# Kernel tuning notes

Measured on AMD Instinct MI355X. Metric: run time of the kernel, lower is better.

Reference implementation:

```python
import jax, jax.numpy as jnp
import numpy as np

M = 0.4
S = 64.0
EPS = 1e-5

def _normalize(x, axis=-1):
    n = jnp.linalg.norm(x, axis=axis, keepdims=True)
    return x / jnp.maximum(n, EPS)

def setup_inputs() -> dict:
    key = jax.random.key(0)
    k1, k2, k3 = jax.random.split(key, 3)
    B, D, C = 512, 512, 100000
    inp = jax.random.normal(k1, (B, D), dtype=jnp.float32)
    weight = jax.random.normal(k2, (C, D), dtype=jnp.float32) * (D ** -0.5)
    label = jax.random.randint(k3, (B,), 0, C, dtype=jnp.int64)
    bias = jnp.full((1,), float(np.log(C * 10)), dtype=jnp.float32)
    return {"input": inp, "label": label, "weight": weight, "bias": bias}

def reference(input, label, weight, bias):
    # cos_theta: [B, C]
    cos_theta = _normalize(input) @ _normalize(weight).T
    cos_m_theta_p = S * (cos_theta - M) - bias
    cos_m_theta_n = S * cos_theta - bias
    # log(1 + exp(x)) with clamp to [-S, S] as in the original
    p_loss = jnp.log1p(jnp.exp(-jnp.clip(cos_m_theta_p, -S, S)))
    n_loss = jnp.log1p(jnp.exp(jnp.clip(cos_m_theta_n, -S, S)))
    one_hot = jax.nn.one_hot(label, cos_theta.shape[1], dtype=jnp.bool_)
    losses = jnp.where(one_hot, p_loss, n_loss)
    return losses.sum(axis=1).mean()
```

## Files before the change

### kernel.cpp

```cpp
#include <hip/hip_runtime.h>
#include <hip/hip_bf16.h>
#include <stdint.h>

#define C_CLS  100000
#define DDIM   512
#define BROWS  512
#define NT     64
#define NSTEP  16
#define EPSN   1e-5f

typedef __attribute__((ext_vector_type(8))) short short8;
typedef __attribute__((ext_vector_type(4))) float f32x4;

__device__ inline unsigned pk2(float a, float b) {
  __hip_bfloat162 h = __float22bfloat162_rn(make_float2(a, b));
  unsigned u; __builtin_memcpy(&u, &h, 4); return u;
}

__global__ void __launch_bounds__(64) k_norm_input(const float* __restrict__ in,
                                                   uint4* __restrict__ xnf,
                                                   float* __restrict__ out) {
  int b = blockIdx.x;
  int lane = threadIdx.x;
  if (b == 0 && lane == 0) out[0] = 0.f;
  const float4* row = (const float4*)(in + b * DDIM);
  float4 v0 = row[lane * 2];
  float4 v1 = row[lane * 2 + 1];
  float ss = v0.x*v0.x + v0.y*v0.y + v0.z*v0.z + v0.w*v0.w
           + v1.x*v1.x + v1.y*v1.y + v1.z*v1.z + v1.w*v1.w;
#pragma unroll
  for (int o = 32; o >= 1; o >>= 1) ss += __shfl_xor(ss, o, 64);
  float sc = 1.f / fmaxf(sqrtf(ss), EPSN);
  uint4 o4;
  o4.x = pk2(v0.x*sc, v0.y*sc);
  o4.y = pk2(v0.z*sc, v0.w*sc);
  o4.z = pk2(v1.x*sc, v1.y*sc);
  o4.w = pk2(v1.z*sc, v1.w*sc);
  int idx = ((lane >> 2) * 32 + (b >> 4)) * 64 + (lane & 3) * 16 + (b & 15);
  xnf[idx] = o4;
}

__global__ void __launch_bounds__(512, 4) k_gemm(const uint4* __restrict__ xnf,
                                                 const float* __restrict__ wt,
                                                 const float* __restrict__ bias,
                                                 float* __restrict__ out) {
  __shared__ __align__(16) unsigned char sW[NSTEP][4096];
  __shared__ float sNsq[NT];
  __shared__ float sRed[8];

  const int tid  = threadIdx.x;
  const int lane = tid & 63;
  const int wv   = tid >> 6;
  const int cbase = blockIdx.x * NT;

  const int cls = tid >> 3;
  const int qb  = tid & 7;
  int wcls = cbase + cls;
  if (wcls >= C_CLS) wcls = C_CLS - 1;
  const float4* wsrc = (const float4*)(wt + (size_t)wcls * DDIM) + qb;

  const int kh_ = (qb >> 1) & 3;
  const int wbyte = (cls >> 4) * 1024 + kh_ * 256
                  + (((cls & 15) * 16) ^ (kh_ << 4)) + (qb & 1) * 8;
  const int rbyte = (lane * 16) ^ (((lane >> 4) & 3) << 4);
  const uint4* abase = xnf + wv * 256 + lane;

  float wsq = 0.f;
#pragma unroll
  for (int h = 0; h < 2; ++h) {
    float4 wr[8];
#pragma unroll
    for (int j = 0; j < 8; ++j) wr[j] = wsrc[(h * 8 + j) * 8];
#pragma unroll
    for (int j = 0; j < 8; ++j) {
      float4 w = wr[j];
      wsq += w.x*w.x + w.y*w.y + w.z*w.z + w.w*w.w;
      uint2 d;
      d.x = pk2(w.x, w.y);
      d.y = pk2(w.z, w.w);
      *(uint2*)(sW[h * 8 + j] + wbyte) = d;
    }
  }
#pragma unroll
  for (int o = 1; o < 8; o <<= 1) wsq += __shfl_xor(wsq, o, 64);
  if (qb == 0) sNsq[cls] = wsq;
  __syncthreads();

  f32x4 acc[4][4];
#pragma unroll
  for (int m = 0; m < 4; m++)
#pragma unroll
    for (int n = 0; n < 4; n++) acc[m][n] = (f32x4)(0.f);

#pragma unroll 1
  for (int s = 0; s < NSTEP; ++s) {
    short8 af[4];
#pragma unroll
    for (int m = 0; m < 4; m++)
      af[m] = *(const short8*)(abase + s * 2048 + m * 64);
    const unsigned char* Wb = sW[s];
#pragma unroll
    for (int n = 0; n < 4; n++) {
      short8 wf = *(const short8*)(Wb + n * 1024 + rbyte);
#pragma unroll
      for (int m = 0; m < 4; m++)
        acc[m][n] = __builtin_amdgcn_mfma_f32_16x16x32_bf16(af[m], wf, acc[m][n], 0, 0, 0);
    }
  }

  const float bv = bias[0];
  float sum = 0.f;
#pragma unroll
  for (int n = 0; n < 4; n++) {
    int cl = n * 16 + (lane & 15);
    float rn = 1.f / fmaxf(sqrtf(sNsq[cl]), EPSN);
    bool valid = (cbase + cl) < C_CLS;
#pragma unroll
    for (int m = 0; m < 4; m++) {
#pragma unroll
      for (int i = 0; i < 4; i++) {
        float cosv = acc[m][n][i] * rn;
        float x = fminf(fmaf(cosv, 64.f, -bv), 64.f);
        float z = __expf(x);
        float l = z * fmaf(z, fmaf(z, 0.33333333f, -0.5f), 1.f);
        if (z > 0.03125f) l = __logf(1.f + z);
        sum += valid ? l : 0.f;
      }
    }
  }
#pragma unroll
  for (int o = 32; o >= 1; o >>= 1) sum += __shfl_xor(sum, o, 64);
  if (lane == 0) sRed[wv] = sum;
  __syncthreads();
  if (tid == 0) {
    float t = 0.f;
#pragma unroll
    for (int i = 0; i < 8; i++) t += sRed[i];
    atomicAdd(out, t * (1.f / 512.f));
  }
}

__global__ void __launch_bounds__(64) k_label(const float* __restrict__ in,
                                              const float* __restrict__ wt,
                                              const int* __restrict__ label,
                                              const float* __restrict__ bias,
                                              float* __restrict__ out) {
  int b = blockIdx.x;
  int lane = threadIdx.x;
  int c = label[b];
  const float4* xr = (const float4*)(in + b * DDIM);
  const float4* wr = (const float4*)(wt + (size_t)c * DDIM);
  float dt = 0.f, sx = 0.f, sw = 0.f;
#pragma unroll
  for (int i = 0; i < 2; i++) {
    float4 x = xr[lane * 2 + i];
    float4 w = wr[lane * 2 + i];
    dt += x.x*w.x + x.y*w.y + x.z*w.z + x.w*w.w;
    sx += x.x*x.x + x.y*x.y + x.z*x.z + x.w*x.w;
    sw += w.x*w.x + w.y*w.y + w.z*w.z + w.w*w.w;
  }
#pragma unroll
  for (int o = 32; o >= 1; o >>= 1) {
    dt += __shfl_xor(dt, o, 64);
    sx += __shfl_xor(sx, o, 64);
    sw += __shfl_xor(sw, o, 64);
  }
  if (lane == 0) {
    float bv = bias[0];
    float cosv = dt / (fmaxf(sqrtf(sx), EPSN) * fmaxf(sqrtf(sw), EPSN));
    float cp = 64.f * (cosv - 0.4f) - bv;
    cp = fminf(fmaxf(cp, -64.f), 64.f);
    float pl = log1pf(expf(-cp));
    float cn = 64.f * cosv - bv;
    cn = fminf(fmaxf(cn, -64.f), 64.f);
    float nl = log1pf(expf(cn));
    atomicAdd(out, (pl - nl) * (1.f / 512.f));
  }
}

extern "C" void kernel_launch(void* const* d_in, const int* in_sizes, int n_in,
                              void* d_out, int out_size, void* d_ws, size_t ws_size,
                              hipStream_t stream) {
  const float* input  = (const float*)d_in[0];
  const int*   label  = (const int*)d_in[1];
  const float* weight = (const float*)d_in[2];
  const float* bias   = (const float*)d_in[3];
  float* out = (float*)d_out;

  uint4* xnf = (uint4*)d_ws;

  k_norm_input<<<BROWS, 64, 0, stream>>>(input, xnf, out);
  k_gemm<<<(C_CLS + NT - 1) / NT, 512, 0, stream>>>(xnf, weight, bias, out);
  k_label<<<BROWS, 64, 0, stream>>>(input, weight, label, bias, out);
}
```

Baseline: 108.9 us.

## Spread atomic accumulation across padded slots and double-buffer A fragment loads

Block partial sums now go into 256 padded workspace slots, and the label terms into 64 more, instead of all blocks doing atomicAdd on one output float. A new final kernel reduces those slots. The GEMM loop now double-buffers the A-fragment global loads across pairs of k-steps and prefetches the first fragment before the weight staging. The epilogue folds the 64 scale into the norm reciprocal, drops the upper clamp, and shortens the log1p polynomial. The aim is to cut atomic contention and hide A load latency, at the cost of an extra kernel launch and slightly different numerics.

```diff
diff --git a/kernel.cpp b/kernel.cpp
--- a/kernel.cpp
+++ b/kernel.cpp
@@ -12,6 +12,7 @@
 typedef __attribute__((ext_vector_type(8))) short short8;
 typedef __attribute__((ext_vector_type(4))) float f32x4;
 
+
 __device__ inline unsigned pk2(float a, float b) {
   __hip_bfloat162 h = __float22bfloat162_rn(make_float2(a, b));
   unsigned u; __builtin_memcpy(&u, &h, 4); return u;
@@ -19,10 +20,13 @@
 
 __global__ void __launch_bounds__(64) k_norm_input(const float* __restrict__ in,
                                                    uint4* __restrict__ xnf,
-                                                   float* __restrict__ out) {
+                                                   float* __restrict__ ws) {
   int b = blockIdx.x;
   int lane = threadIdx.x;
-  if (b == 0 && lane == 0) out[0] = 0.f;
+  if (lane == 0) {
+    if (b < 256) ws[b * 16] = 0.f;
+    else if (b < 320) ws[4096 + (b - 256) * 16] = 0.f;
+  }
   const float4* row = (const float4*)(in + b * DDIM);
   float4 v0 = row[lane * 2];
   float4 v1 = row[lane * 2 + 1];
@@ -43,7 +47,7 @@
 __global__ void __launch_bounds__(512, 4) k_gemm(const uint4* __restrict__ xnf,
                                                  const float* __restrict__ wt,
                                                  const float* __restrict__ bias,
-                                                 float* __restrict__ out) {
+                                                 float* __restrict__ ws) {
   __shared__ __align__(16) unsigned char sW[NSTEP][4096];
   __shared__ float sNsq[NT];
   __shared__ float sRed[8];
@@ -52,33 +56,44 @@
   const int lane = tid & 63;
   const int wv   = tid >> 6;
   const int cbase = blockIdx.x * NT;
+
+  const int rbyte = (lane * 16) ^ (((lane >> 4) & 3) << 4);
+  const uint4* abase = xnf + wv * 256 + lane;
+
+  short8 afA[4], afB[4];
+#pragma unroll
+  for (int m = 0; m < 4; m++)
+    afA[m] = *(const short8*)(abase + m * 64);
 
   const int cls = tid >> 3;
   const int qb  = tid & 7;
   int wcls = cbase + cls;
   if (wcls >= C_CLS) wcls = C_CLS - 1;
   const float4* wsrc = (const float4*)(wt + (size_t)wcls * DDIM) + qb;
-
   const int kh_ = (qb >> 1) & 3;
   const int wbyte = (cls >> 4) * 1024 + kh_ * 256
                   + (((cls & 15) * 16) ^ (kh_ << 4)) + (qb & 1) * 8;
-  const int rbyte = (lane * 16) ^ (((lane >> 4) & 3) << 4);
-  const uint4* abase = xnf + wv * 256 + lane;
 
   float wsq = 0.f;
-#pragma unroll
-  for (int h = 0; h < 2; ++h) {
-    float4 wr[8];
-#pragma unroll
-    for (int j = 0; j < 8; ++j) wr[j] = wsrc[(h * 8 + j) * 8];
+  {
+    float4 wr0[8], wr1[8];
+#pragma unroll
+    for (int j = 0; j < 8; ++j) wr0[j] = wsrc[j * 8];
+#pragma unroll
+    for (int j = 0; j < 8; ++j) wr1[j] = wsrc[(8 + j) * 8];
 #pragma unroll
     for (int j = 0; j < 8; ++j) {
-      float4 w = wr[j];
+      float4 w = wr0[j];
       wsq += w.x*w.x + w.y*w.y + w.z*w.z + w.w*w.w;
-      uint2 d;
-      d.x = pk2(w.x, w.y);
-      d.y = pk2(w.z, w.w);
-      *(uint2*)(sW[h * 8 + j] + wbyte) = d;
+      uint2 d; d.x = pk2(w.x, w.y); d.y = pk2(w.z, w.w);
+      *(uint2*)(sW[j] + wbyte) = d;
+    }
+#pragma unroll
+    for (int j = 0; j < 8; ++j) {
+      float4 w = wr1[j];
+      wsq += w.x*w.x + w.y*w.y + w.z*w.z + w.w*w.w;
+      uint2 d; d.x = pk2(w.x, w.y); d.y = pk2(w.z, w.w);
+      *(uint2*)(sW[8 + j] + wbyte) = d;
     }
   }
 #pragma unroll
@@ -92,12 +107,12 @@
 #pragma unroll
     for (int n = 0; n < 4; n++) acc[m][n] = (f32x4)(0.f);
 
-#pragma unroll 1
-  for (int s = 0; s < NSTEP; ++s) {
-    short8 af[4];
+  auto loadA = [&](short8* af, int s) {
 #pragma unroll
     for (int m = 0; m < 4; m++)
       af[m] = *(const short8*)(abase + s * 2048 + m * 64);
+  };
+  auto compute = [&](int s, const short8* af) {
     const unsigned char* Wb = sW[s];
 #pragma unroll
     for (int n = 0; n < 4; n++) {
@@ -106,6 +121,15 @@
       for (int m = 0; m < 4; m++)
         acc[m][n] = __builtin_amdgcn_mfma_f32_16x16x32_bf16(af[m], wf, acc[m][n], 0, 0, 0);
     }
+  };
+
+#pragma unroll 1
+  for (int s2 = 0; s2 < NSTEP / 2; ++s2) {
+    int s0 = s2 * 2;
+    loadA(afB, s0 + 1);
+    compute(s0, afA);
+    if (s2 < NSTEP / 2 - 1) loadA(afA, s0 + 2);
+    compute(s0 + 1, afB);
   }
 
   const float bv = bias[0];
@@ -113,16 +137,15 @@
 #pragma unroll
   for (int n = 0; n < 4; n++) {
     int cl = n * 16 + (lane & 15);
-    float rn = 1.f / fmaxf(sqrtf(sNsq[cl]), EPSN);
+    float s64 = 64.f / fmaxf(sqrtf(sNsq[cl]), EPSN);
     bool valid = (cbase + cl) < C_CLS;
 #pragma unroll
     for (int m = 0; m < 4; m++) {
 #pragma unroll
       for (int i = 0; i < 4; i++) {
-        float cosv = acc[m][n][i] * rn;
-        float x = fminf(fmaf(cosv, 64.f, -bv), 64.f);
+        float x = fmaf(acc[m][n][i], s64, -bv);
         float z = __expf(x);
-        float l = z * fmaf(z, fmaf(z, 0.33333333f, -0.5f), 1.f);
+        float l = fmaf(-0.5f * z, z, z);
         if (z > 0.03125f) l = __logf(1.f + z);
         sum += valid ? l : 0.f;
       }
@@ -136,7 +159,7 @@
     float t = 0.f;
 #pragma unroll
     for (int i = 0; i < 8; i++) t += sRed[i];
-    atomicAdd(out, t * (1.f / 512.f));
+    atomicAdd(&ws[(blockIdx.x & 255) * 16], t);
   }
 }
 
@@ -144,7 +167,7 @@
                                               const float* __restrict__ wt,
                                               const int* __restrict__ label,
                                               const float* __restrict__ bias,
-                                              float* __restrict__ out) {
+                                              float* __restrict__ ws) {
   int b = blockIdx.x;
   int lane = threadIdx.x;
   int c = label[b];
@@ -174,8 +197,19 @@
     float cn = 64.f * cosv - bv;
     cn = fminf(fmaxf(cn, -64.f), 64.f);
     float nl = log1pf(expf(cn));
-    atomicAdd(out, (pl - nl) * (1.f / 512.f));
-  }
+    atomicAdd(&ws[4096 + (b & 63) * 16], pl - nl);
+  }
+}
+
+__global__ void __launch_bounds__(64) k_final(const float* __restrict__ ws,
+                                              float* __restrict__ out) {
+  int lane = threadIdx.x;
+  float s = ws[lane * 16] + ws[(lane + 64) * 16]
+          + ws[(lane + 128) * 16] + ws[(lane + 192) * 16]
+          + ws[4096 + lane * 16];
+#pragma unroll
+  for (int o = 32; o >= 1; o >>= 1) s += __shfl_xor(s, o, 64);
+  if (lane == 0) out[0] = s * (1.f / 512.f);
 }
 
 extern "C" void kernel_launch(void* const* d_in, const int* in_sizes, int n_in,
@@ -186,10 +220,11 @@
   const float* weight = (const float*)d_in[2];
   const float* bias   = (const float*)d_in[3];
   float* out = (float*)d_out;
-
-  uint4* xnf = (uint4*)d_ws;
-
-  k_norm_input<<<BROWS, 64, 0, stream>>>(input, xnf, out);
-  k_gemm<<<(C_CLS + NT - 1) / NT, 512, 0, stream>>>(xnf, weight, bias, out);
-  k_label<<<BROWS, 64, 0, stream>>>(input, weight, label, bias, out);
-}
+  float* ws  = (float*)d_ws;
+  uint4* xnf = (uint4*)((char*)d_ws + 32768);
+
+  k_norm_input<<<BROWS, 64, 0, stream>>>(input, xnf, ws);
+  k_gemm<<<(C_CLS + NT - 1) / NT, 512, 0, stream>>>(xnf, weight, bias, ws);
+  k_label<<<BROWS, 64, 0, stream>>>(input, weight, label, bias, ws);
+  k_final<<<1, 64, 0, stream>>>(ws, out);
+}
```

After: 96.89 us. 1.12x faster.
